# Optimization experiments

Hardware: AMD Instinct MI355X
Metric: run time of the kernel (lower is better)

The kernel has to match this reference:

```python
import jax, jax.numpy as jnp
import numpy as np

DIM = 1024
HEADS = 16
HD = DIM // HEADS          # 64
HID = 4 * DIM              # 4096
TPF = 1374                 # tokens_per_frame
LR = 0.1
NS_ITERS = 5
TTT_STEPS = 2
B, S = 2, 4
SN = S * TPF               # 5496


def _newton_schulz(G, iters=NS_ITERS):
    """Muon Newton-Schulz orthogonalization (quintic iteration)."""
    a, b, c = 3.4445, -4.7750, 2.0315
    X = G / (jnp.linalg.norm(G) + 1e-7)
    transposed = G.shape[0] > G.shape[1]
    if transposed:
        X = X.T
    for _ in range(iters):
        A = X @ X.T                      # [m,m], m = min(rows, cols)
        X = a * X + (b * A + c * (A @ A)) @ X
    return X.T if transposed else X


def _muon_update(p, g):
    return p - LR * _newton_schulz(g)


def setup_inputs() -> dict:
    key = jax.random.key(0)
    ks = jax.random.split(key, 8)
    inp = {
        "x": jax.random.normal(ks[0], (B, SN, DIM), jnp.float32),
        "qkv_w": jax.random.normal(ks[1], (DIM, 3 * DIM), jnp.float32) * (DIM ** -0.5),
        "qkv_b": jnp.zeros((3 * DIM,), jnp.float32),
        "qn_scale": jnp.ones((HD,), jnp.float32),
        "qn_bias": jnp.zeros((HD,), jnp.float32),
        "kn_scale": jnp.ones((HD,), jnp.float32),
        "kn_bias": jnp.zeros((HD,), jnp.float32),
        # theta: lecun-normal scale (std = 1/sqrt(fan_in))
        "ttt_gate": jax.random.normal(ks[2], (DIM, HID), jnp.float32) * (DIM ** -0.5),
        "ttt_val": jax.random.normal(ks[3], (DIM, HID), jnp.float32) * (DIM ** -0.5),
        "ttt_proj": jax.random.normal(ks[4], (HID, DIM), jnp.float32) * (HID ** -0.5),
        "proj_w": jax.random.normal(ks[5], (DIM, DIM), jnp.float32) * (DIM ** -0.5),
        "proj_b": jnp.zeros((DIM,), jnp.float32),
    }
    return inp


def reference(x, qkv_w, qkv_b, qn_scale, qn_bias, kn_scale, kn_bias,
              ttt_gate, ttt_val, ttt_proj, proj_w, proj_b):
    Bx, SNx, _ = x.shape
    qkv = x @ qkv_w + qkv_b                       # [B, SN, 3*DIM]
    q, k, v = jnp.split(qkv, 3, axis=-1)
    q = q.reshape(Bx, SNx, HEADS, HD)
    k = k.reshape(Bx, SNx, HEADS, HD)
    # per-head L2 normalize then affine NormLayer (x*scale + bias)
    q = q / (jnp.linalg.norm(q, axis=-1, keepdims=True) + 1e-6) * qn_scale + qn_bias
    k = k / (jnp.linalg.norm(k, axis=-1, keepdims=True) + 1e-6) * kn_scale + kn_bias
    q_ttt = q.reshape(-1, DIM)                    # [B*SN, DIM]
    k_ttt = k.reshape(-1, DIM)
    # no short_conv param at init -> v_mixed is identity, so v_target == v
    v_ttt = v.reshape(-1, DIM)

    theta = {"gate": ttt_gate, "val": ttt_val, "proj": ttt_proj}

    def loss_fn(p):
        h = jax.nn.swish(k_ttt @ p["gate"]) * (k_ttt @ p["val"])   # [B*SN, HID]
        pred = h @ p["proj"]                                        # [B*SN, DIM]
        return jnp.mean((pred - v_ttt) ** 2)

    for _ in range(TTT_STEPS):
        grads = jax.grad(loss_fn)(theta)
        theta = {kk: _muon_update(theta[kk], grads[kk]) for kk in theta}

    h_q = jax.nn.swish(q_ttt @ theta["gate"]) * (q_ttt @ theta["val"])
    o = (h_q @ theta["proj"]) @ proj_w + proj_b
    return o.reshape(Bx, SNx, DIM)
```

## Files before the change

### kernel.cpp

```cpp
#include <hip/hip_runtime.h>
#include <stdint.h>

#define NTOK 10992
#define NTOKA 11264
#define CHK 1408
#define NCH 8
#define FCHK 5632
#define PMi 4194304

typedef unsigned short u16;
typedef __attribute__((ext_vector_type(8))) __bf16 b8;
typedef __attribute__((ext_vector_type(4))) float f32x4;

__device__ __forceinline__ u16 f2b(float f) {
  union { float f; uint32_t u; } v; v.f = f;
  return (u16)((v.u + 0x7fffu + ((v.u >> 16) & 1u)) >> 16);
}
__device__ __forceinline__ float b2f(u16 b) {
  union { uint32_t u; float f; } v; v.u = ((uint32_t)b) << 16; return v.f;
}
__device__ __forceinline__ uint2 pk4(u16 a, u16 b, u16 c, u16 d) {
  uint2 r; r.x = (uint32_t)a | ((uint32_t)b << 16); r.y = (uint32_t)c | ((uint32_t)d << 16);
  return r;
}
__device__ __forceinline__ void gload16(const u16* g, u16* l) {
  __builtin_amdgcn_global_load_lds((const __attribute__((address_space(1))) void*)(const void*)g,
                                   (__attribute__((address_space(3))) void*)(void*)l, 16, 0, 0);
}

struct GA {
  const u16* A[3]; const u16* B[3];
  void* C[3]; u16* O1[3]; u16* OT[3];
  const void* E0[3]; const u16* E1[3];
  int lda[3], ldb[3];
  int M, N, K, ldc, ldo1, ldt, lde0, lde1;
  float p0, p1;
};

template <int EPI, int SPLIT>
__global__ __launch_bounds__(256, 2) void gemm_bt(GA g) {
  __shared__ u16 As[128 * 32];
  __shared__ u16 Bs[128 * 32];
  int bz = blockIdx.z, koff = 0, klen = g.K;
  if constexpr (SPLIT) { koff = (bz & 1) * (g.K >> 1); bz >>= 1; klen = g.K >> 1; }
  const u16* __restrict__ A = g.A[bz] + koff;
  const u16* __restrict__ B = g.B[bz] + koff;
  const int lda = g.lda[bz], ldb = g.ldb[bz];
  const int m0 = blockIdx.y * 128, n0 = blockIdx.x * 128;
  const int tid = threadIdx.x, w = tid >> 6, lane = tid & 63;
  const int wr = (w >> 1) * 64, wc = (w & 1) * 64;
  const int ln = lane & 15, lq = lane >> 4;

  f32x4 acc[4][4];
#pragma unroll
  for (int i = 0; i < 4; ++i)
#pragma unroll
    for (int j = 0; j < 4; ++j)
#pragma unroll
      for (int r = 0; r < 4; ++r) acc[i][j][r] = 0.f;

  const u16* Ag = A + (size_t)(m0 + 32 * w + (lane >> 2)) * lda + (lane & 3) * 8;
  const u16* Bg = B + (size_t)(n0 + 32 * w + (lane >> 2)) * ldb + (lane & 3) * 8;
  u16* AsW = &As[w * 1024];
  u16* BsW = &Bs[w * 1024];
  const int nkt = klen >> 5;

  for (int kt = 0; kt < nkt; ++kt) {
    __syncthreads();
    gload16(Ag, AsW);
    gload16(Ag + (size_t)16 * lda, AsW + 512);
    gload16(Bg, BsW);
    gload16(Bg + (size_t)16 * ldb, BsW + 512);
    Ag += 32; Bg += 32;
    __syncthreads();
    b8 af[4], bfr[4];
#pragma unroll
    for (int i = 0; i < 4; ++i) af[i] = *(const b8*)&As[(wr + i * 16 + ln) * 32 + lq * 8];
#pragma unroll
    for (int j = 0; j < 4; ++j) bfr[j] = *(const b8*)&Bs[(wc + j * 16 + ln) * 32 + lq * 8];
#pragma unroll
    for (int i = 0; i < 4; ++i)
#pragma unroll
      for (int j = 0; j < 4; ++j)
        acc[i][j] = __builtin_amdgcn_mfma_f32_16x16x32_bf16(af[i], bfr[j], acc[i][j], 0, 0, 0);
  }

  float* Cf = (float*)g.C[bz];
  u16* Cb = (u16*)g.C[bz];
  u16* O1 = g.O1[bz];
  u16* OT = g.OT[bz];
  const float* E0f = (const float*)g.E0[bz];
  const u16* E0b = (const u16*)g.E0[bz];
  const u16* E1b = g.E1[bz];

#pragma unroll
  for (int i = 0; i < 4; ++i) {
    const int mb = m0 + wr + i * 16 + lq * 4;
    if (mb >= g.M) continue;
#pragma unroll
    for (int j = 0; j < 4; ++j) {
      const int n = n0 + wc + j * 16 + ln;
      if (n >= g.N) continue;
      float vv[4];
#pragma unroll
      for (int r = 0; r < 4; ++r) vv[r] = acc[i][j][r];
      if constexpr (EPI == 0) {
#pragma unroll
        for (int r = 0; r < 4; ++r) Cb[(size_t)(mb + r) * g.ldc + n] = f2b(vv[r]);
      } else if constexpr (EPI == 1) {
        const float bias = E0f[n];
#pragma unroll
        for (int r = 0; r < 4; ++r) Cb[(size_t)(mb + r) * g.ldc + n] = f2b(vv[r] + bias);
      } else if constexpr (EPI == 3) {
        u16 oq[4];
#pragma unroll
        for (int r = 0; r < 4; ++r) {
          const int m = mb + r;
          Cb[(size_t)m * g.ldc + n] = f2b(vv[r]);
          const float zg = b2f(E0b[(size_t)m * g.lde0 + n]);
          const float s = 1.f / (1.f + __expf(-zg));
          const u16 ub = f2b(zg * s * vv[r]);
          O1[(size_t)m * g.ldo1 + n] = ub;
          oq[r] = ub;
        }
        *(uint2*)&OT[(size_t)n * g.ldt + mb] = pk4(oq[0], oq[1], oq[2], oq[3]);
      } else if constexpr (EPI == 4) {
#pragma unroll
        for (int r = 0; r < 4; ++r) {
          const int m = mb + r;
          const float zg = b2f(E0b[(size_t)m * g.lde0 + n]);
          const float s = 1.f / (1.f + __expf(-zg));
          Cb[(size_t)m * g.ldc + n] = f2b(zg * s * vv[r]);
        }
      } else if constexpr (EPI == 5) {
        u16 cq[4], oq[4];
#pragma unroll
        for (int r = 0; r < 4; ++r) {
          const int m = mb + r;
          const float zg = b2f(E0b[(size_t)m * g.lde0 + n]);
          const float zv = b2f(E1b[(size_t)m * g.lde1 + n]);
          const float s = 1.f / (1.f + __expf(-zg));
          cq[r] = f2b(vv[r] * zv * s * (1.f + zg * (1.f - s)));
          oq[r] = f2b(vv[r] * zg * s);
        }
        *(uint2*)&Cb[(size_t)n * g.ldt + mb] = pk4(cq[0], cq[1], cq[2], cq[3]);
        *(uint2*)&O1[(size_t)n * g.ldt + mb] = pk4(oq[0], oq[1], oq[2], oq[3]);
      } else if constexpr (EPI == 6) {
        const float bias = E0f[n];
#pragma unroll
        for (int r = 0; r < 4; ++r) Cf[(size_t)(mb + r) * g.ldc + n] = vv[r] + bias;
      } else if constexpr (EPI == 8) {
#pragma unroll
        for (int r = 0; r < 4; ++r) atomicAdd(&Cf[(size_t)(mb + r) * g.ldc + n], vv[r]);
      } else if constexpr (EPI == 9) {
        u16 cq[4];
#pragma unroll
        for (int r = 0; r < 4; ++r) {
          const int m = mb + r;
          const u16 ub = f2b(g.p0 * b2f(E0b[(size_t)m * g.lde0 + n]) + vv[r]);
          Cb[(size_t)m * g.ldc + n] = ub;
          cq[r] = ub;
        }
        *(uint2*)&OT[(size_t)n * g.ldt + mb] = pk4(cq[0], cq[1], cq[2], cq[3]);
      }
    }
  }
}

template <int EPI>
__global__ __launch_bounds__(256, 2) void gemm64(GA g) {
  __shared__ u16 As[64 * 32];
  __shared__ u16 Bs[64 * 32];
  const int bz = blockIdx.z;
  const u16* __restrict__ A = g.A[bz];
  const u16* __restrict__ B = g.B[bz];
  const int lda = g.lda[bz], ldb = g.ldb[bz];
  const int m0 = blockIdx.y * 64, n0 = blockIdx.x * 64;
  const int tid = threadIdx.x, w = tid >> 6, lane = tid & 63;
  const int wr = (w >> 1) * 32, wc = (w & 1) * 32;
  const int ln = lane & 15, lq = lane >> 4;

  f32x4 acc[2][2];
#pragma unroll
  for (int i = 0; i < 2; ++i)
#pragma unroll
    for (int j = 0; j < 2; ++j)
#pragma unroll
      for (int r = 0; r < 4; ++r) acc[i][j][r] = 0.f;

  const u16* Ag = A + (size_t)(m0 + 16 * w + (lane >> 2)) * lda + (lane & 3) * 8;
  const u16* Bg = B + (size_t)(n0 + 16 * w + (lane >> 2)) * ldb + (lane & 3) * 8;
  u16* AsW = &As[w * 512];
  u16* BsW = &Bs[w * 512];
  const int nkt = g.K >> 5;

  for (int kt = 0; kt < nkt; ++kt) {
    __syncthreads();
    gload16(Ag, AsW);
    gload16(Bg, BsW);
    Ag += 32; Bg += 32;
    __syncthreads();
    b8 af[2], bfr[2];
#pragma unroll
    for (int i = 0; i < 2; ++i) af[i] = *(const b8*)&As[(wr + i * 16 + ln) * 32 + lq * 8];
#pragma unroll
    for (int j = 0; j < 2; ++j) bfr[j] = *(const b8*)&Bs[(wc + j * 16 + ln) * 32 + lq * 8];
#pragma unroll
    for (int i = 0; i < 2; ++i)
#pragma unroll
      for (int j = 0; j < 2; ++j)
        acc[i][j] = __builtin_amdgcn_mfma_f32_16x16x32_bf16(af[i], bfr[j], acc[i][j], 0, 0, 0);
  }

  float* Cf = (float*)g.C[bz];
  u16* Cb = (u16*)g.C[bz];
  u16* OT = g.OT[bz];
  const float* E0f = (const float*)g.E0[bz];
  const u16* E0b = (const u16*)g.E0[bz];

#pragma unroll
  for (int i = 0; i < 2; ++i) {
    const int mb = m0 + wr + i * 16 + lq * 4;
    if (mb >= g.M) continue;
#pragma unroll
    for (int j = 0; j < 2; ++j) {
      const int n = n0 + wc + j * 16 + ln;
      if (n >= g.N) continue;
      float vv[4];
#pragma unroll
      for (int r = 0; r < 4; ++r) vv[r] = acc[i][j][r];
      if constexpr (EPI == 0) {
#pragma unroll
        for (int r = 0; r < 4; ++r) Cb[(size_t)(mb + r) * g.ldc + n] = f2b(vv[r]);
      } else if constexpr (EPI == 2) {
        u16 cq[4];
#pragma unroll
        for (int r = 0; r < 4; ++r) {
          const int m = mb + r;
          const u16 ub = f2b((vv[r] - b2f(E0b[(size_t)m * g.lde0 + n])) * g.p0);
          Cb[(size_t)m * g.ldc + n] = ub;
          cq[r] = ub;
        }
        *(uint2*)&OT[(size_t)n * g.ldt + mb] = pk4(cq[0], cq[1], cq[2], cq[3]);
      } else if constexpr (EPI == 6) {
        const float bias = E0f[n];
#pragma unroll
        for (int r = 0; r < 4; ++r) Cf[(size_t)(mb + r) * g.ldc + n] = vv[r] + bias;
      } else if constexpr (EPI == 7) {
#pragma unroll
        for (int r = 0; r < 4; ++r) {
          const int m = mb + r;
          Cb[(size_t)m * g.ldc + n] =
              f2b(g.p0 * b2f(E0b[(size_t)m * g.lde0 + n]) + g.p1 * vv[r]);
        }
      }
    }
  }
}

__global__ __launch_bounds__(256) void norm_qkv(const u16* __restrict__ qkvB,
    const float* __restrict__ qs, const float* __restrict__ qbi,
    const float* __restrict__ ks, const float* __restrict__ kbi,
    u16* __restrict__ qb, u16* __restrict__ kb, u16* __restrict__ vb) {
  const int tok = blockIdx.x;
  const int t = threadIdx.x;
  const int d = t * 4;
  const u16* row = qkvB + (size_t)tok * 3072;
  const uint2 qu = *(const uint2*)(row + d);
  const uint2 ku = *(const uint2*)(row + 1024 + d);
  *(uint2*)(vb + (size_t)tok * 1024 + d) = *(const uint2*)(row + 2048 + d);
  float q0 = b2f(qu.x & 0xffff), q1 = b2f(qu.x >> 16), q2 = b2f(qu.y & 0xffff), q3 = b2f(qu.y >> 16);
  float k0 = b2f(ku.x & 0xffff), k1 = b2f(ku.x >> 16), k2 = b2f(ku.y & 0xffff), k3 = b2f(ku.y >> 16);
  float sq = q0 * q0 + q1 * q1 + q2 * q2 + q3 * q3;
  float sk = k0 * k0 + k1 * k1 + k2 * k2 + k3 * k3;
  for (int off = 1; off < 16; off <<= 1) { sq += __shfl_xor(sq, off); sk += __shfl_xor(sk, off); }
  const float rq = 1.f / (sqrtf(sq) + 1e-6f);
  const float rk = 1.f / (sqrtf(sk) + 1e-6f);
  const int hd = d & 63;
  const float4 qsv = *(const float4*)(qs + hd);
  const float4 qbv = *(const float4*)(qbi + hd);
  const float4 ksv = *(const float4*)(ks + hd);
  const float4 kbv = *(const float4*)(kbi + hd);
  uint64_t pq = (uint64_t)f2b(q0 * rq * qsv.x + qbv.x)
              | ((uint64_t)f2b(q1 * rq * qsv.y + qbv.y) << 16)
              | ((uint64_t)f2b(q2 * rq * qsv.z + qbv.z) << 32)
              | ((uint64_t)f2b(q3 * rq * qsv.w + qbv.w) << 48);
  uint64_t pk = (uint64_t)f2b(k0 * rk * ksv.x + kbv.x)
              | ((uint64_t)f2b(k1 * rk * ksv.y + kbv.y) << 16)
              | ((uint64_t)f2b(k2 * rk * ksv.z + kbv.z) << 32)
              | ((uint64_t)f2b(k3 * rk * ksv.w + kbv.w) << 48);
  *(uint64_t*)(qb + (size_t)tok * 1024 + d) = pq;
  *(uint64_t*)(kb + (size_t)tok * 1024 + d) = pk;
}

__global__ __launch_bounds__(256) void tr_b16(const u16* __restrict__ in, u16* __restrict__ out,
                                              int Cin, int Rtot, int Rval,
                                              size_t inStr, size_t outStr) {
  const int b = blockIdx.z;
  in += (size_t)b * inStr; out += (size_t)b * outStr;
  __shared__ u16 t[32][33];
  const int c0 = blockIdx.x * 32, r0 = blockIdx.y * 32;
  const int tx = threadIdx.x, ty = threadIdx.y;
#pragma unroll
  for (int yy = 0; yy < 4; ++yy) {
    const int rr = ty * 4 + yy;
    const int r = r0 + rr;
    t[rr][tx] = (r < Rval) ? in[(size_t)r * Cin + c0 + tx] : (u16)0;
  }
  __syncthreads();
#pragma unroll
  for (int yy = 0; yy < 4; ++yy) {
    const int cc = ty * 4 + yy;
    out[(size_t)(c0 + cc) * Rtot + r0 + tx] = t[tx][cc];
  }
}

__global__ __launch_bounds__(256) void tr_f32b(const float* __restrict__ in, u16* __restrict__ out,
                                               int Cin, int Rtot) {
  __shared__ u16 t[32][33];
  const int c0 = blockIdx.x * 32, r0 = blockIdx.y * 32;
  const int tx = threadIdx.x, ty = threadIdx.y;
#pragma unroll
  for (int yy = 0; yy < 4; ++yy) {
    const int rr = ty * 4 + yy;
    t[rr][tx] = f2b(in[(size_t)(r0 + rr) * Cin + c0 + tx]);
  }
  __syncthreads();
#pragma unroll
  for (int yy = 0; yy < 4; ++yy) {
    const int cc = ty * 4 + yy;
    out[(size_t)(c0 + cc) * Rtot + r0 + tx] = t[tx][cc];
  }
}

__global__ void cvt_k(const float* __restrict__ in, u16* __restrict__ out, int n) {
  const int i = blockIdx.x * 256 + threadIdx.x;
  if (i < n) out[i] = f2b(in[i]);
}

__global__ void diag_k(float* __restrict__ out, int n, float val) {
  const int i = blockIdx.x * 256 + threadIdx.x;
  if (i < n) out[i] = val;
}

__global__ __launch_bounds__(256) void sumsq_k(const float* __restrict__ g, float* __restrict__ out) {
  const int b = blockIdx.y;
  const float* p = g + (size_t)b * PMi;
  float s = 0.f;
  for (int i = blockIdx.x * 256 + threadIdx.x; i < PMi; i += gridDim.x * 256) {
    float v = p[i]; s += v * v;
  }
  for (int off = 32; off > 0; off >>= 1) s += __shfl_xor(s, off);
  __shared__ float red[4];
  if ((threadIdx.x & 63) == 0) red[threadIdx.x >> 6] = s;
  __syncthreads();
  if (threadIdx.x == 0) atomicAdd(out + b, red[0] + red[1] + red[2] + red[3]);
}

__global__ __launch_bounds__(256) void scale_k(const float* __restrict__ g, const float* __restrict__ ss,
                                               u16* __restrict__ Xb) {
  const int b = blockIdx.y;
  const float r = 1.f / (sqrtf(ss[b]) + 1e-7f);
  const size_t o = (size_t)b * PMi;
  for (int i = blockIdx.x * 256 + threadIdx.x; i < PMi; i += gridDim.x * 256)
    Xb[o + i] = f2b(g[o + i] * r);
}

__global__ __launch_bounds__(256) void muon_apply(const u16* __restrict__ Xb_,
    u16* __restrict__ Gt, u16* __restrict__ Vt, u16* __restrict__ Pt, u16* __restrict__ Pb) {
  const int b = blockIdx.z;
  __shared__ float xs[32][33];
  __shared__ u16 ns[32][33];
  const int j0 = blockIdx.x * 32;
  const int i0 = blockIdx.y * 32;
  const u16* X = Xb_ + (size_t)b * PMi;
  const int tx = threadIdx.x, ty = threadIdx.y;
#pragma unroll
  for (int yy = 0; yy < 4; ++yy) {
    const int r = ty * 4 + yy;
    xs[r][tx] = b2f(X[(size_t)(i0 + r) * 4096 + j0 + tx]);
  }
  __syncthreads();
  if (b < 2) {
    u16* T = b ? Vt : Gt;
#pragma unroll
    for (int yy = 0; yy < 4; ++yy) {
      const int rr = ty * 4 + yy;
      const size_t idx = (size_t)(j0 + rr) * 1024 + i0 + tx;
      T[idx] = f2b(b2f(T[idx]) - 0.1f * xs[tx][rr]);
    }
  } else {
#pragma unroll
    for (int yy = 0; yy < 4; ++yy) {
      const int rr = ty * 4 + yy;
      const size_t idx = (size_t)(j0 + rr) * 1024 + i0 + tx;
      const float nv = b2f(Pb[idx]) - 0.1f * xs[tx][rr];
      const u16 nb = f2b(nv);
      Pb[idx] = nb;
      ns[rr][tx] = nb;
    }
    __syncthreads();
#pragma unroll
    for (int yy = 0; yy < 4; ++yy) {
      const int rr = ty * 4 + yy;
      Pt[(size_t)(i0 + rr) * 4096 + j0 + tx] = ns[tx][rr];
    }
  }
}

static GA mk(const u16* A, const u16* B, void* C, int M, int N, int K,
             int lda, int ldb, int ldc) {
  GA a{};
  a.A[0] = a.A[1] = a.A[2] = A;
  a.B[0] = a.B[1] = a.B[2] = B;
  a.C[0] = a.C[1] = a.C[2] = C;
  a.lda[0] = a.lda[1] = a.lda[2] = lda;
  a.ldb[0] = a.ldb[1] = a.ldb[2] = ldb;
  a.M = M; a.N = N; a.K = K; a.ldc = ldc;
  return a;
}

extern "C" void kernel_launch(void* const* d_in, const int* in_sizes, int n_in,
                              void* d_out, int out_size, void* d_ws, size_t ws_size,
                              hipStream_t stream) {
  (void)in_sizes; (void)n_in;
  const float* x      = (const float*)d_in[0];
  const float* qkv_w  = (const float*)d_in[1];
  const float* qkv_b  = (const float*)d_in[2];
  const float* qn_s   = (const float*)d_in[3];
  const float* qn_b   = (const float*)d_in[4];
  const float* kn_s   = (const float*)d_in[5];
  const float* kn_b   = (const float*)d_in[6];
  const float* g_gate = (const float*)d_in[7];
  const float* g_val  = (const float*)d_in[8];
  const float* g_proj = (const float*)d_in[9];
  const float* proj_w = (const float*)d_in[10];
  const float* proj_b = (const float*)d_in[11];
  float* out = (float*)d_out;

  const size_t PM = PMi;
  const size_t TD = (size_t)NTOKA * 1024;

  const size_t NEED = 253231360 + 4096;
  if (ws_size < NEED) {
    diag_k<<<dim3((out_size + 255) / 256), dim3(256), 0, stream>>>(out, out_size,
                                                                   (float)(ws_size >> 20));
    return;
  }

  char* p = (char*)d_ws;
  auto carve = [&](size_t bytes) { char* r = p; p += (bytes + 255) & ~(size_t)255; return (void*)r; };
  auto cdiv = [](int a, int b) { return (a + b - 1) / b; };

  u16* Gt     = (u16*)carve(PM * 2);
  u16* Vt     = (u16*)carve(PM * 2);
  u16* Pt     = (u16*)carve(PM * 2);
  u16* Pb     = (u16*)carve(PM * 2);
  u16* projWt = (u16*)carve(1048576ull * 2);
  u16* qb     = (u16*)carve(TD * 2);
  u16* kb     = (u16*)carve(TD * 2);
  u16* vT     = (u16*)carve(TD * 2);
  u16* kT     = (u16*)carve(TD * 2);
  float* ssq  = (float*)carve(256);
  char* arena = p;

  u16* xb     = (u16*)arena;
  u16* qkvWt  = (u16*)(arena + 23068672);
  u16* qkvB   = (u16*)(arena + 29360128);
  u16* vb_tmp = (u16*)(arena + 96894976);
  u16* zg     = (u16*)arena;
  u16* zv     = (u16*)(arena + 11534336);
  u16* hh     = (u16*)(arena + 23068672);
  u16* hT     = (u16*)(arena + 34603008);
  u16* dzgT   = (u16*)(arena + 46137344);
  u16* dzvT   = (u16*)(arena + 57671680);
  u16* dpredT = (u16*)(arena + 69206016);
  u16* dpredb = (u16*)(arena + 72089600);
  float* gAll = (float*)(arena + 74973184);
  u16* XAb  = (u16*)arena;
  u16* XAbT = (u16*)(arena + 25165824);
  u16* XBb  = (u16*)(arena + 50331648);
  u16* XBbT = (u16*)(arena + 75497472);
  u16* Ab   = (u16*)(arena + 100663296);
  u16* Wb   = (u16*)(arena + 106954752);
  u16* zgc = (u16*)arena;
  u16* oc  = (u16*)(arena + 46137344);

  const dim3 blk(256), tb32(32, 8);
  const float inv2 = 2.0f / (10992.0f * 1024.0f);
  const float nsa = 3.4445f, nsb = -4.7750f, nsc = 2.0315f;

  cvt_k<<<dim3(43968), blk, 0, stream>>>(x, xb, NTOK * 1024);
  cvt_k<<<dim3(16384), blk, 0, stream>>>(g_proj, Pb, (int)PM);
  tr_f32b<<<dim3(96, 32), tb32, 0, stream>>>(qkv_w, qkvWt, 3072, 1024);
  tr_f32b<<<dim3(32, 32), tb32, 0, stream>>>(proj_w, projWt, 1024, 1024);
  tr_f32b<<<dim3(128, 32), tb32, 0, stream>>>(g_gate, Gt, 4096, 1024);
  tr_f32b<<<dim3(128, 32), tb32, 0, stream>>>(g_val, Vt, 4096, 1024);
  tr_f32b<<<dim3(32, 128), tb32, 0, stream>>>(g_proj, Pt, 1024, 4096);

  {
    GA a = mk(xb, qkvWt, qkvB, NTOK, 3072, 1024, 1024, 1024, 3072);
    a.E0[0] = a.E0[1] = a.E0[2] = qkv_b;
    gemm_bt<1, 0><<<dim3(24, 86, 1), blk, 0, stream>>>(a);
  }
  norm_qkv<<<dim3(NTOK), blk, 0, stream>>>(qkvB, qn_s, qn_b, kn_s, kn_b, qb, kb, vb_tmp);
  tr_b16<<<dim3(32, 352, 1), tb32, 0, stream>>>(kb, kT, 1024, NTOKA, NTOK, 0, 0);
  tr_b16<<<dim3(32, 352, 1), tb32, 0, stream>>>(vb_tmp, vT, 1024, NTOKA, NTOK, 0, 0);

  for (int step = 0; step < 2; ++step) {
    hipMemsetAsync(gAll, 0, 3 * PM * 4, stream);
    for (int c = 0; c < NCH; ++c) {
      const int c0 = c * CHK;
      const int vc = (NTOK - c0 < CHK) ? (NTOK - c0) : CHK;
      const int mt = cdiv(vc, 128);
      const u16* kc = kb + (size_t)c0 * 1024;
      if (vc < CHK)
        hipMemsetAsync(hT, 0, 37486592, stream);
      gemm_bt<0, 0><<<dim3(32, mt, 1), blk, 0, stream>>>(
          mk(kc, Gt, zg, vc, 4096, 1024, 1024, 1024, 4096));
      {
        GA a = mk(kc, Vt, zv, vc, 4096, 1024, 1024, 1024, 4096);
        a.O1[0] = hh; a.ldo1 = 4096; a.OT[0] = hT; a.ldt = CHK;
        a.E0[0] = zg; a.lde0 = 4096;
        gemm_bt<3, 0><<<dim3(32, mt, 1), blk, 0, stream>>>(a);
      }
      {
        GA a = mk(Pt, hh, dpredT, 1024, vc, 4096, 4096, 4096, CHK);
        a.OT[0] = dpredb; a.ldt = 1024;
        a.E0[0] = vT + c0; a.lde0 = NTOKA; a.p0 = inv2;
        gemm64<2><<<dim3(cdiv(vc, 64), 16, 1), blk, 0, stream>>>(a);
      }
      {
        GA a = mk(dpredb, Pb, dzgT, vc, 4096, 1024, 1024, 1024, 0);
        a.O1[0] = dzvT; a.ldt = CHK;
        a.E0[0] = zg; a.lde0 = 4096; a.E1[0] = zv; a.lde1 = 4096;
        gemm_bt<5, 0><<<dim3(32, mt, 1), blk, 0, stream>>>(a);
      }
      {
        GA a{};
        a.A[0] = kT + c0; a.A[1] = kT + c0; a.A[2] = dpredT;
        a.lda[0] = NTOKA; a.lda[1] = NTOKA; a.lda[2] = CHK;
        a.B[0] = dzgT; a.B[1] = dzvT; a.B[2] = hT;
        a.ldb[0] = a.ldb[1] = a.ldb[2] = CHK;
        a.C[0] = gAll; a.C[1] = gAll + PM; a.C[2] = gAll + 2 * PM;
        a.M = 1024; a.N = 4096; a.K = CHK; a.ldc = 4096;
        gemm_bt<8, 1><<<dim3(32, 8, 6), blk, 0, stream>>>(a);
      }
    }
    hipMemsetAsync(ssq, 0, 16, stream);
    sumsq_k<<<dim3(512, 3), blk, 0, stream>>>(gAll, ssq);
    scale_k<<<dim3(2048, 3), blk, 0, stream>>>(gAll, ssq, XAb);
    tr_b16<<<dim3(128, 32, 3), tb32, 0, stream>>>(XAb, XAbT, 4096, 1024, 1024, PM, PM);

    u16* Xi_b = XAb; u16* Xi_bT = XAbT;
    u16* Xo_b = XBb; u16* Xo_bT = XBbT;
    for (int it = 0; it < 5; ++it) {
      {
        GA a{};
        for (int b = 0; b < 3; ++b) {
          a.A[b] = Xi_b + (size_t)b * PM; a.B[b] = Xi_b + (size_t)b * PM;
          a.C[b] = Ab + (size_t)b * 1048576;
          a.lda[b] = 4096; a.ldb[b] = 4096;
        }
        a.M = 1024; a.N = 1024; a.K = 4096; a.ldc = 1024;
        gemm64<0><<<dim3(16, 16, 3), blk, 0, stream>>>(a);
      }
      {
        GA a{};
        for (int b = 0; b < 3; ++b) {
          a.A[b] = Ab + (size_t)b * 1048576; a.B[b] = Ab + (size_t)b * 1048576;
          a.C[b] = Wb + (size_t)b * 1048576; a.E0[b] = Ab + (size_t)b * 1048576;
          a.lda[b] = 1024; a.ldb[b] = 1024;
        }
        a.M = 1024; a.N = 1024; a.K = 1024; a.ldc = 1024; a.lde0 = 1024;
        a.p0 = nsb; a.p1 = nsc;
        gemm64<7><<<dim3(16, 16, 3), blk, 0, stream>>>(a);
      }
      {
        GA a{};
        for (int b = 0; b < 3; ++b) {
          a.A[b] = Wb + (size_t)b * 1048576; a.B[b] = Xi_bT + (size_t)b * PM;
          a.C[b] = Xo_b + (size_t)b * PM; a.OT[b] = Xo_bT + (size_t)b * PM;
          a.E0[b] = Xi_b + (size_t)b * PM;
          a.lda[b] = 1024; a.ldb[b] = 1024;
        }
        a.M = 1024; a.N = 4096; a.K = 1024; a.ldc = 4096; a.ldt = 1024;
        a.lde0 = 4096; a.p0 = nsa;
        gemm_bt<9, 0><<<dim3(32, 8, 3), blk, 0, stream>>>(a);
      }
      u16* tb = Xi_b; Xi_b = Xo_b; Xo_b = tb;
      u16* tt = Xi_bT; Xi_bT = Xo_bT; Xo_bT = tt;
    }
    muon_apply<<<dim3(128, 32, 3), tb32, 0, stream>>>(Xi_b, Gt, Vt, Pt, Pb);
  }

  for (int fc = 0; fc < 2; ++fc) {
    const int c0 = fc * FCHK;
    const int vc = (NTOK - c0 < FCHK) ? (NTOK - c0) : FCHK;
    const int mt = cdiv(vc, 128), mt64 = cdiv(vc, 64);
    const u16* qc = qb + (size_t)c0 * 1024;
    gemm_bt<0, 0><<<dim3(32, mt, 1), blk, 0, stream>>>(
        mk(qc, Gt, zgc, vc, 4096, 1024, 1024, 1024, 4096));
    {
      GA a = mk(qc, Vt, zgc, vc, 4096, 1024, 1024, 1024, 4096);
      a.E0[0] = zgc; a.lde0 = 4096;
      gemm_bt<4, 0><<<dim3(32, mt, 1), blk, 0, stream>>>(a);
    }
    gemm64<0><<<dim3(16, mt64, 1), blk, 0, stream>>>(
        mk(zgc, Pt, oc, vc, 1024, 4096, 4096, 4096, 1024));
    {
      GA a = mk(oc, projWt, out + (size_t)c0 * 1024, vc, 1024, 1024, 1024, 1024, 1024);
      a.E0[0] = proj_b;
      gemm64<6><<<dim3(16, mt64, 1), blk, 0, stream>>>(a);
    }
  }
}
```

Baseline: 6.730 ms.

## Double TTT gradient chunk size when workspace allows, reuse hh buffer for dzgT

When the workspace is large enough, the TTT gradient loop now processes token chunks of 2816 instead of 1408, halving the number of chunk iterations and the split-K weight-gradient GEMM passes that accumulate into gAll. To fit the larger chunk in the arena, the hh buffer is reused as the dzgT output once it is no longer needed, and the buffer offsets are computed from the chunk size. Larger chunks cut launch count and repeated read-modify-write of the fp32 gradient accumulators. The cost is a bigger workspace footprint and extra memsets on the partial final chunk.

After: 6.673 ms. About the same (-0.8%).

```diff
diff --git a/kernel.cpp b/kernel.cpp
--- a/kernel.cpp
+++ b/kernel.cpp
@@ -3,8 +3,6 @@
 
 #define NTOK 10992
 #define NTOKA 11264
-#define CHK 1408
-#define NCH 8
 #define FCHK 5632
 #define PMi 4194304
 
@@ -441,12 +439,14 @@
   const size_t PM = PMi;
   const size_t TD = (size_t)NTOKA * 1024;
 
-  const size_t NEED = 253231360 + 4096;
-  if (ws_size < NEED) {
+  const size_t NEED1 = 253231360 + 4096;
+  const size_t NEED2 = 127926528 + 177209344 + 4096;
+  if (ws_size < NEED1) {
     diag_k<<<dim3((out_size + 255) / 256), dim3(256), 0, stream>>>(out, out_size,
                                                                    (float)(ws_size >> 20));
     return;
   }
+  const int CHKr = (ws_size >= NEED2) ? 2816 : 1408;
 
   char* p = (char*)d_ws;
   auto carve = [&](size_t bytes) { char* r = p; p += (bytes + 255) & ~(size_t)255; return (void*)r; };
@@ -468,15 +468,16 @@
   u16* qkvWt  = (u16*)(arena + 23068672);
   u16* qkvB   = (u16*)(arena + 29360128);
   u16* vb_tmp = (u16*)(arena + 96894976);
+  const size_t CB = (size_t)CHKr * 4096 * 2;
+  const size_t DP = (size_t)CHKr * 1024 * 2;
   u16* zg     = (u16*)arena;
-  u16* zv     = (u16*)(arena + 11534336);
-  u16* hh     = (u16*)(arena + 23068672);
-  u16* hT     = (u16*)(arena + 34603008);
-  u16* dzgT   = (u16*)(arena + 46137344);
-  u16* dzvT   = (u16*)(arena + 57671680);
-  u16* dpredT = (u16*)(arena + 69206016);
-  u16* dpredb = (u16*)(arena + 72089600);
-  float* gAll = (float*)(arena + 74973184);
+  u16* zv     = (u16*)(arena + CB);
+  u16* hh     = (u16*)(arena + 2 * CB);
+  u16* hT     = (u16*)(arena + 3 * CB);
+  u16* dzvT   = (u16*)(arena + 4 * CB);
+  u16* dpredT = (u16*)(arena + 5 * CB);
+  u16* dpredb = (u16*)(arena + 5 * CB + DP);
+  float* gAll = (float*)(arena + 5 * CB + 2 * DP);
   u16* XAb  = (u16*)arena;
   u16* XAbT = (u16*)(arena + 25165824);
   u16* XBb  = (u16*)(arena + 50331648);
@@ -509,41 +510,42 @@
 
   for (int step = 0; step < 2; ++step) {
     hipMemsetAsync(gAll, 0, 3 * PM * 4, stream);
-    for (int c = 0; c < NCH; ++c) {
-      const int c0 = c * CHK;
-      const int vc = (NTOK - c0 < CHK) ? (NTOK - c0) : CHK;
+    for (int c0 = 0; c0 < NTOK; c0 += CHKr) {
+      const int vc = (NTOK - c0 < CHKr) ? (NTOK - c0) : CHKr;
       const int mt = cdiv(vc, 128);
       const u16* kc = kb + (size_t)c0 * 1024;
-      if (vc < CHK)
-        hipMemsetAsync(hT, 0, 37486592, stream);
+      if (vc < CHKr)
+        hipMemsetAsync(hT, 0, 2 * CB + DP, stream);
       gemm_bt<0, 0><<<dim3(32, mt, 1), blk, 0, stream>>>(
           mk(kc, Gt, zg, vc, 4096, 1024, 1024, 1024, 4096));
       {
         GA a = mk(kc, Vt, zv, vc, 4096, 1024, 1024, 1024, 4096);
-        a.O1[0] = hh; a.ldo1 = 4096; a.OT[0] = hT; a.ldt = CHK;
+        a.O1[0] = hh; a.ldo1 = 4096; a.OT[0] = hT; a.ldt = CHKr;
         a.E0[0] = zg; a.lde0 = 4096;
         gemm_bt<3, 0><<<dim3(32, mt, 1), blk, 0, stream>>>(a);
       }
       {
-        GA a = mk(Pt, hh, dpredT, 1024, vc, 4096, 4096, 4096, CHK);
+        GA a = mk(Pt, hh, dpredT, 1024, vc, 4096, 4096, 4096, CHKr);
         a.OT[0] = dpredb; a.ldt = 1024;
         a.E0[0] = vT + c0; a.lde0 = NTOKA; a.p0 = inv2;
         gemm64<2><<<dim3(cdiv(vc, 64), 16, 1), blk, 0, stream>>>(a);
       }
+      if (vc < CHKr)
+        hipMemsetAsync(hh, 0, CB, stream);
       {
-        GA a = mk(dpredb, Pb, dzgT, vc, 4096, 1024, 1024, 1024, 0);
-        a.O1[0] = dzvT; a.ldt = CHK;
+        GA a = mk(dpredb, Pb, hh, vc, 4096, 1024, 1024, 1024, 0);
+        a.O1[0] = dzvT; a.ldt = CHKr;
         a.E0[0] = zg; a.lde0 = 4096; a.E1[0] = zv; a.lde1 = 4096;
         gemm_bt<5, 0><<<dim3(32, mt, 1), blk, 0, stream>>>(a);
       }
       {
         GA a{};
         a.A[0] = kT + c0; a.A[1] = kT + c0; a.A[2] = dpredT;
-        a.lda[0] = NTOKA; a.lda[1] = NTOKA; a.lda[2] = CHK;
-        a.B[0] = dzgT; a.B[1] = dzvT; a.B[2] = hT;
-        a.ldb[0] = a.ldb[1] = a.ldb[2] = CHK;
+        a.lda[0] = NTOKA; a.lda[1] = NTOKA; a.lda[2] = CHKr;
+        a.B[0] = hh; a.B[1] = dzvT; a.B[2] = hT;
+        a.ldb[0] = a.ldb[1] = a.ldb[2] = CHKr;
         a.C[0] = gAll; a.C[1] = gAll + PM; a.C[2] = gAll + 2 * PM;
-        a.M = 1024; a.N = 4096; a.K = CHK; a.ldc = 4096;
+        a.M = 1024; a.N = 4096; a.K = CHKr; a.ldc = 4096;
         gemm_bt<8, 1><<<dim3(32, 8, 6), blk, 0, stream>>>(a);
       }
     }
```
